# Kernel tuning notes

Hardware: AMD Instinct MI355X
Metric: run time of the kernel (lower is better)

Reference implementation:

```python
import jax, jax.numpy as jnp
import numpy as np

N_NODES = 100000
N_EDGES = 1600000
IN_FEATS = 16
HIDDEN = 100
OUT_FEATS = 3


def setup_inputs() -> dict:
    key = jax.random.key(0)
    ks = jax.random.split(key, 12)
    inp = {
        "x": jax.random.normal(ks[0], (N_NODES, IN_FEATS), dtype=jnp.float32),
        "edge_feats": jax.random.uniform(ks[1], (N_EDGES, 1), dtype=jnp.float32),
        "src": jax.random.randint(ks[2], (N_EDGES,), 0, N_NODES, dtype=jnp.int32),
        "dst": jax.random.randint(ks[3], (N_EDGES,), 0, N_NODES, dtype=jnp.int32),
        # lift: Linear(in_feats, hidden)
        "W_lift": jax.random.normal(ks[4], (IN_FEATS, HIDDEN), dtype=jnp.float32) / np.sqrt(IN_FEATS),
        "b_lift": jnp.zeros((HIDDEN,), dtype=jnp.float32),
        # three MPL layers: Linear(2*hidden, hidden)
        "W1": jax.random.normal(ks[5], (2 * HIDDEN, HIDDEN), dtype=jnp.float32) / np.sqrt(2 * HIDDEN),
        "b1": jnp.zeros((HIDDEN,), dtype=jnp.float32),
        "W2": jax.random.normal(ks[6], (2 * HIDDEN, HIDDEN), dtype=jnp.float32) / np.sqrt(2 * HIDDEN),
        "b2": jnp.zeros((HIDDEN,), dtype=jnp.float32),
        "W3": jax.random.normal(ks[7], (2 * HIDDEN, HIDDEN), dtype=jnp.float32) / np.sqrt(2 * HIDDEN),
        "b3": jnp.zeros((HIDDEN,), dtype=jnp.float32),
        # out: Linear(hidden, out_feats)
        "W_out": jax.random.normal(ks[8], (HIDDEN, OUT_FEATS), dtype=jnp.float32) / np.sqrt(HIDDEN),
        "b_out": jnp.zeros((OUT_FEATS,), dtype=jnp.float32),
    }
    return inp


def _mpl(h, edge_feats, src, dst, W, b):
    # gather src node feats, multiply by per-edge weight, scatter-sum to dst
    msg = h[src] * edge_feats                                # [E, H]
    reduced = jax.ops.segment_sum(msg, dst, num_segments=N_NODES)  # [N, H]
    return jax.nn.relu(jnp.concatenate([h, reduced], axis=-1) @ W + b)


def reference(x, edge_feats, src, dst, W_lift, b_lift, W1, b1, W2, b2, W3, b3, W_out, b_out):
    h = jnp.tanh(x @ W_lift + b_lift)          # [N, 100]
    h = _mpl(h, edge_feats, src, dst, W1, b1)
    h = _mpl(h, edge_feats, src, dst, W2, b2)
    h = _mpl(h, edge_feats, src, dst, W3, b3)
    return jax.nn.sigmoid(h @ W_out + b_out)   # [N, 3]
```

## Files before the change

kernel.cpp:

```cpp
#include <hip/hip_runtime.h>
#include <hip/hip_fp16.h>
#include <cstdint>
#include <cstddef>

#define NN 100000
#define NE 1600000
#define HID 100
#define INF 16

typedef _Float16 f16x8 __attribute__((ext_vector_type(8)));
typedef float f32x4 __attribute__((ext_vector_type(4)));

__device__ __forceinline__ float2 up_f16(unsigned int u) {
  __half2 h = *reinterpret_cast<const __half2*>(&u);
  return __half22float2(h);
}
__device__ __forceinline__ unsigned int pk_f16(float lo, float hi) {
  __half2 h = __floats2half2_rn(lo, hi);
  return *reinterpret_cast<const unsigned int*>(&h);
}
__device__ __forceinline__ f16x8 as_f16x8(uint4 v) {
  union { uint4 u; f16x8 f; } c; c.u = v; return c.f;
}

__global__ void k_hist(const int* __restrict__ dst, int* __restrict__ deg,
                       int* __restrict__ rank) {
  int e = blockIdx.x * 256 + threadIdx.x;
  if (e < NE) rank[e] = atomicAdd(&deg[dst[e]], 1);
}

__global__ void k_scan1(const int* __restrict__ deg, int* __restrict__ offs,
                        int* __restrict__ bsum) {
  __shared__ int s[256];
  int t = threadIdx.x;
  int i = blockIdx.x * 256 + t;
  int v = (i < NN) ? deg[i] : 0;
  s[t] = v; __syncthreads();
  for (int off = 1; off < 256; off <<= 1) {
    int x = (t >= off) ? s[t - off] : 0;
    __syncthreads();
    s[t] += x;
    __syncthreads();
  }
  if (i < NN) offs[i] = s[t] - v;
  if (t == 255) bsum[blockIdx.x] = s[255];
}

__global__ void k_scan2(int* __restrict__ bsum, int nb) {
  __shared__ int s[512];
  int t = threadIdx.x;
  int v = (t < nb) ? bsum[t] : 0;
  s[t] = v; __syncthreads();
  for (int off = 1; off < 512; off <<= 1) {
    int x = (t >= off) ? s[t - off] : 0;
    __syncthreads();
    s[t] += x;
    __syncthreads();
  }
  if (t < nb) bsum[t] = s[t] - v;
}

__global__ void k_scan3(int* __restrict__ offs, const int* __restrict__ bsum) {
  int i = blockIdx.x * 256 + threadIdx.x;
  if (i < NN) offs[i] += bsum[i >> 8];
  else if (i == NN) offs[NN] = NE;
}

__global__ void k_fill(const int* __restrict__ src, const int* __restrict__ dst,
                       const float* __restrict__ ef, const int* __restrict__ offs,
                       const int* __restrict__ rank,
                       unsigned long long* __restrict__ epack) {
  int e = blockIdx.x * 256 + threadIdx.x;
  if (e >= NE) return;
  int p = offs[dst[e]] + rank[e];
  unsigned long long v = (unsigned int)src[e] |
                         ((unsigned long long)(unsigned int)__float_as_int(ef[e]) << 32);
  epack[p] = v;
}

__device__ __forceinline__ float wval(const float* W, int kp, int col) {
  if (col >= HID) return 0.f;
  if (kp < 128) return (kp < 100) ? W[kp * HID + col] : 0.f;
  int k2 = kp - 128;
  return (k2 < 100) ? W[(100 + k2) * HID + col] : 0.f;
}
__global__ void k_wpack(const float* __restrict__ W, uint4* __restrict__ Bp) {
  int tid = blockIdx.x * 256 + threadIdx.x;
  if (tid >= 56 * 64) return;
  int lane = tid & 63, f = tid >> 6;
  int s = f / 7, n = f % 7;
  int col = n * 16 + (lane & 15);
  int kb = s * 32 + (lane >> 4) * 8;
  unsigned int u0 = pk_f16(wval(W, kb + 0, col), wval(W, kb + 1, col));
  unsigned int u1 = pk_f16(wval(W, kb + 2, col), wval(W, kb + 3, col));
  unsigned int u2 = pk_f16(wval(W, kb + 4, col), wval(W, kb + 5, col));
  unsigned int u3 = pk_f16(wval(W, kb + 6, col), wval(W, kb + 7, col));
  Bp[tid] = make_uint4(u0, u1, u2, u3);
}

__global__ __launch_bounds__(256) void k_lift(const float* __restrict__ x,
                                              const float* __restrict__ Wl,
                                              const float* __restrict__ bl,
                                              unsigned short* __restrict__ h16) {
  __shared__ uint2 sh[256][25];
  int t = threadIdx.x;
  int n = blockIdx.x * 256 + t;
  int nc = n < NN ? n : NN - 1;
  const float4* W4 = (const float4*)Wl;
  const float4* b4 = (const float4*)bl;
  float4 acc[25];
  #pragma unroll
  for (int j = 0; j < 25; ++j) acc[j] = b4[j];
  const float4* xr = (const float4*)(x + (size_t)nc * INF);
  for (int k4 = 0; k4 < 4; ++k4) {
    float4 xv = xr[k4];
    #pragma unroll
    for (int c = 0; c < 4; ++c) {
      float xs = (&xv.x)[c];
      int k = k4 * 4 + c;
      #pragma unroll
      for (int j = 0; j < 25; ++j) {
        acc[j].x = fmaf(xs, W4[k * 25 + j].x, acc[j].x);
        acc[j].y = fmaf(xs, W4[k * 25 + j].y, acc[j].y);
        acc[j].z = fmaf(xs, W4[k * 25 + j].z, acc[j].z);
        acc[j].w = fmaf(xs, W4[k * 25 + j].w, acc[j].w);
      }
    }
  }
  #pragma unroll
  for (int j = 0; j < 25; ++j) {
    float4 v = acc[j];
    sh[t][j] = make_uint2(pk_f16(tanhf(v.x), tanhf(v.y)),
                          pk_f16(tanhf(v.z), tanhf(v.w)));
  }
  __syncthreads();
  const uint4* shv = (const uint4*)sh;
  uint4* ov = (uint4*)h16;
  size_t gbase = (size_t)blockIdx.x * 3200;
  #pragma unroll
  for (int i = 0; i < 13; ++i) {
    int idx = i * 256 + t;
    if (idx < 3200 && gbase + idx < 1250000) ov[gbase + idx] = shv[idx];
  }
}

__global__ __launch_bounds__(256) void k_reduce(const unsigned short* __restrict__ h16,
                                                const int* __restrict__ offs,
                                                const int2* __restrict__ ep,
                                                unsigned int* __restrict__ red16) {
  int wid = (blockIdx.x * 256 + threadIdx.x) >> 6;
  int node = __builtin_amdgcn_readfirstlane(wid);
  int lane = threadIdx.x & 63;
  int lc = lane < 25 ? lane : 24;
  int beg = offs[node], end = offs[node + 1];
  const uint2* __restrict__ h2 = (const uint2*)h16;
  float4 acc = make_float4(0.f, 0.f, 0.f, 0.f);
  int i = beg;
  for (; i + 8 <= end; i += 8) {
    int2 e0 = ep[i + 0], e1 = ep[i + 1], e2 = ep[i + 2], e3 = ep[i + 3];
    int2 e4 = ep[i + 4], e5 = ep[i + 5], e6 = ep[i + 6], e7 = ep[i + 7];
    uint2 v0 = h2[(size_t)e0.x * 25 + lc];
    uint2 v1 = h2[(size_t)e1.x * 25 + lc];
    uint2 v2 = h2[(size_t)e2.x * 25 + lc];
    uint2 v3 = h2[(size_t)e3.x * 25 + lc];
    uint2 v4 = h2[(size_t)e4.x * 25 + lc];
    uint2 v5 = h2[(size_t)e5.x * 25 + lc];
    uint2 v6 = h2[(size_t)e6.x * 25 + lc];
    uint2 v7 = h2[(size_t)e7.x * 25 + lc];
    float w0 = __int_as_float(e0.y), w1 = __int_as_float(e1.y);
    float w2 = __int_as_float(e2.y), w3 = __int_as_float(e3.y);
    float w4 = __int_as_float(e4.y), w5 = __int_as_float(e5.y);
    float w6 = __int_as_float(e6.y), w7 = __int_as_float(e7.y);
    float2 a0 = up_f16(v0.x), b0 = up_f16(v0.y);
    float2 a1 = up_f16(v1.x), b1 = up_f16(v1.y);
    float2 a2 = up_f16(v2.x), b2 = up_f16(v2.y);
    float2 a3 = up_f16(v3.x), b3 = up_f16(v3.y);
    float2 a4 = up_f16(v4.x), b4 = up_f16(v4.y);
    float2 a5 = up_f16(v5.x), b5 = up_f16(v5.y);
    float2 a6 = up_f16(v6.x), b6 = up_f16(v6.y);
    float2 a7 = up_f16(v7.x), b7 = up_f16(v7.y);
    acc.x = fmaf(w0, a0.x, acc.x); acc.y = fmaf(w0, a0.y, acc.y);
    acc.z = fmaf(w0, b0.x, acc.z); acc.w = fmaf(w0, b0.y, acc.w);
    acc.x = fmaf(w1, a1.x, acc.x); acc.y = fmaf(w1, a1.y, acc.y);
    acc.z = fmaf(w1, b1.x, acc.z); acc.w = fmaf(w1, b1.y, acc.w);
    acc.x = fmaf(w2, a2.x, acc.x); acc.y = fmaf(w2, a2.y, acc.y);
    acc.z = fmaf(w2, b2.x, acc.z); acc.w = fmaf(w2, b2.y, acc.w);
    acc.x = fmaf(w3, a3.x, acc.x); acc.y = fmaf(w3, a3.y, acc.y);
    acc.z = fmaf(w3, b3.x, acc.z); acc.w = fmaf(w3, b3.y, acc.w);
    acc.x = fmaf(w4, a4.x, acc.x); acc.y = fmaf(w4, a4.y, acc.y);
    acc.z = fmaf(w4, b4.x, acc.z); acc.w = fmaf(w4, b4.y, acc.w);
    acc.x = fmaf(w5, a5.x, acc.x); acc.y = fmaf(w5, a5.y, acc.y);
    acc.z = fmaf(w5, b5.x, acc.z); acc.w = fmaf(w5, b5.y, acc.w);
    acc.x = fmaf(w6, a6.x, acc.x); acc.y = fmaf(w6, a6.y, acc.y);
    acc.z = fmaf(w6, b6.x, acc.z); acc.w = fmaf(w6, b6.y, acc.w);
    acc.x = fmaf(w7, a7.x, acc.x); acc.y = fmaf(w7, a7.y, acc.y);
    acc.z = fmaf(w7, b7.x, acc.z); acc.w = fmaf(w7, b7.y, acc.w);
  }
  for (; i + 4 <= end; i += 4) {
    int2 e0 = ep[i + 0], e1 = ep[i + 1], e2 = ep[i + 2], e3 = ep[i + 3];
    uint2 v0 = h2[(size_t)e0.x * 25 + lc];
    uint2 v1 = h2[(size_t)e1.x * 25 + lc];
    uint2 v2 = h2[(size_t)e2.x * 25 + lc];
    uint2 v3 = h2[(size_t)e3.x * 25 + lc];
    float w0 = __int_as_float(e0.y), w1 = __int_as_float(e1.y);
    float w2 = __int_as_float(e2.y), w3 = __int_as_float(e3.y);
    float2 a0 = up_f16(v0.x), b0 = up_f16(v0.y);
    float2 a1 = up_f16(v1.x), b1 = up_f16(v1.y);
    float2 a2 = up_f16(v2.x), b2 = up_f16(v2.y);
    float2 a3 = up_f16(v3.x), b3 = up_f16(v3.y);
    acc.x = fmaf(w0, a0.x, acc.x); acc.y = fmaf(w0, a0.y, acc.y);
    acc.z = fmaf(w0, b0.x, acc.z); acc.w = fmaf(w0, b0.y, acc.w);
    acc.x = fmaf(w1, a1.x, acc.x); acc.y = fmaf(w1, a1.y, acc.y);
    acc.z = fmaf(w1, b1.x, acc.z); acc.w = fmaf(w1, b1.y, acc.w);
    acc.x = fmaf(w2, a2.x, acc.x); acc.y = fmaf(w2, a2.y, acc.y);
    acc.z = fmaf(w2, b2.x, acc.z); acc.w = fmaf(w2, b2.y, acc.w);
    acc.x = fmaf(w3, a3.x, acc.x); acc.y = fmaf(w3, a3.y, acc.y);
    acc.z = fmaf(w3, b3.x, acc.z); acc.w = fmaf(w3, b3.y, acc.w);
  }
  for (; i < end; ++i) {
    int2 e0 = ep[i];
    uint2 v0 = h2[(size_t)e0.x * 25 + lc];
    float w0 = __int_as_float(e0.y);
    float2 a0 = up_f16(v0.x), b0 = up_f16(v0.y);
    acc.x = fmaf(w0, a0.x, acc.x); acc.y = fmaf(w0, a0.y, acc.y);
    acc.z = fmaf(w0, b0.x, acc.z); acc.w = fmaf(w0, b0.y, acc.w);
  }
  if (lane < 25) {
    ((uint2*)red16)[(size_t)node * 25 + lane] =
        make_uint2(pk_f16(acc.x, acc.y), pk_f16(acc.z, acc.w));
  }
}

__global__ __launch_bounds__(256) void k_mlp(const unsigned int* __restrict__ hp,
                                             const unsigned int* __restrict__ rp,
                                             const uint4* __restrict__ Bpk,
                                             const float* __restrict__ bias,
                                             unsigned short* __restrict__ out16) {
  __shared__ unsigned int xs[64 * 132];
  const int t = threadIdx.x;
  const int w = t >> 6, lane = t & 63;
  const int blk = blockIdx.x;
  const size_t base2 = (size_t)blk * 3200;
  const size_t limit2 = (size_t)NN * 50;

  for (int i = t; i < 64 * 28; i += 256) {
    int row = i / 28, c = i % 28;
    int col = (c < 14) ? (50 + c) : (100 + c);
    xs[row * 132 + col] = 0;
  }
  for (int i = t; i < 3200; i += 256) {
    int row = i / 50, c = i % 50;
    size_t g = base2 + i; if (g >= limit2) g = limit2 - 1;
    xs[row * 132 + c] = hp[g];
    xs[row * 132 + 64 + c] = rp[g];
  }
  __syncthreads();

  const int rowA = (w << 4) + (lane & 15);
  const int kg = lane >> 4;
  f32x4 acc[7];
  #pragma unroll
  for (int n = 0; n < 7; ++n) {
    int c = n * 16 + (lane & 15);
    float bv = (c < HID) ? bias[c] : 0.f;
    acc[n] = (f32x4){bv, bv, bv, bv};
  }
  const uint4* bp = Bpk + lane;
  #pragma unroll
  for (int s = 0; s < 8; ++s) {
    uint4 av = *reinterpret_cast<const uint4*>(&xs[rowA * 132 + s * 16 + kg * 4]);
    f16x8 af = as_f16x8(av);
    #pragma unroll
    for (int n = 0; n < 7; ++n) {
      f16x8 bf = as_f16x8(bp[(s * 7 + n) * 64]);
      acc[n] = __builtin_amdgcn_mfma_f32_16x16x32_f16(af, bf, acc[n], 0, 0, 0);
    }
  }
  const int orow0 = blk * 64 + (w << 4) + (kg << 2);
  const int ocol = lane & 15;
  #pragma unroll
  for (int n = 0; n < 7; ++n) {
    int c = n * 16 + ocol;
    if (c < HID) {
      #pragma unroll
      for (int q = 0; q < 4; ++q) {
        int rr = orow0 + q;
        if (rr < NN) {
          float v = fmaxf(acc[n][q], 0.f);
          out16[(size_t)rr * HID + c] = __half_as_ushort(__float2half(v));
        }
      }
    }
  }
}

__global__ __launch_bounds__(256) void k_out(const unsigned short* __restrict__ h16,
                                             const float* __restrict__ Wo,
                                             const float* __restrict__ bo,
                                             float* __restrict__ out) {
  int n = blockIdx.x * 256 + threadIdx.x;
  if (n >= NN) return;
  float a0 = bo[0], a1 = bo[1], a2 = bo[2];
  const uint2* hr = (const uint2*)(h16 + (size_t)n * HID);
  for (int k2 = 0; k2 < 25; ++k2) {
    uint2 v = hr[k2];
    float2 fa = up_f16(v.x), fb = up_f16(v.y);
    int k = k2 * 4;
    a0 = fmaf(fa.x, Wo[(k + 0) * 3 + 0], a0); a1 = fmaf(fa.x, Wo[(k + 0) * 3 + 1], a1); a2 = fmaf(fa.x, Wo[(k + 0) * 3 + 2], a2);
    a0 = fmaf(fa.y, Wo[(k + 1) * 3 + 0], a0); a1 = fmaf(fa.y, Wo[(k + 1) * 3 + 1], a1); a2 = fmaf(fa.y, Wo[(k + 1) * 3 + 2], a2);
    a0 = fmaf(fb.x, Wo[(k + 2) * 3 + 0], a0); a1 = fmaf(fb.x, Wo[(k + 2) * 3 + 1], a1); a2 = fmaf(fb.x, Wo[(k + 2) * 3 + 2], a2);
    a0 = fmaf(fb.y, Wo[(k + 3) * 3 + 0], a0); a1 = fmaf(fb.y, Wo[(k + 3) * 3 + 1], a1); a2 = fmaf(fb.y, Wo[(k + 3) * 3 + 2], a2);
  }
  out[(size_t)n * 3 + 0] = 1.f / (1.f + expf(-a0));
  out[(size_t)n * 3 + 1] = 1.f / (1.f + expf(-a1));
  out[(size_t)n * 3 + 2] = 1.f / (1.f + expf(-a2));
}

extern "C" void kernel_launch(void* const* d_in, const int* in_sizes, int n_in,
                              void* d_out, int out_size, void* d_ws, size_t ws_size,
                              hipStream_t stream) {
  const float* x  = (const float*)d_in[0];
  const float* ef = (const float*)d_in[1];
  const int*   src = (const int*)d_in[2];
  const int*   dst = (const int*)d_in[3];
  const float* Wl = (const float*)d_in[4];
  const float* bl = (const float*)d_in[5];
  const float* W1 = (const float*)d_in[6];
  const float* b1 = (const float*)d_in[7];
  const float* W2 = (const float*)d_in[8];
  const float* b2 = (const float*)d_in[9];
  const float* W3 = (const float*)d_in[10];
  const float* b3 = (const float*)d_in[11];
  const float* Wo = (const float*)d_in[12];
  const float* bo = (const float*)d_in[13];
  float* out = (float*)d_out;

  char* ws = (char*)d_ws;
  unsigned int*   red16  = (unsigned int*)(ws);
  uint4*          Wpk    = (uint4*)(ws + 20000000);
  unsigned short* hA16   = (unsigned short*)(ws + 40000000);
  unsigned short* hB16   = (unsigned short*)(ws + 60000000);
  int*            offs   = (int*)(ws + 80000000);
  int*            deg    = (int*)(ws + 80400128);
  unsigned long long* epack = (unsigned long long*)(ws + 80800256);
  int*            bsum   = (int*)(ws + 93600256);
  int*            rank   = (int*)ws;

  const int scanBlocks = (NN + 255) / 256;
  const int mlpBlocks  = (NN + 63) / 64;
  uint4* Wpk1 = Wpk;
  uint4* Wpk2 = Wpk + 3584;
  uint4* Wpk3 = Wpk + 7168;

  hipMemsetAsync(deg, 0, NN * sizeof(int), stream);
  k_hist <<<(NE + 255) / 256, 256, 0, stream>>>(dst, deg, rank);
  k_scan1<<<scanBlocks, 256, 0, stream>>>(deg, offs, bsum);
  k_scan2<<<1, 512, 0, stream>>>(bsum, scanBlocks);
  k_scan3<<<scanBlocks, 256, 0, stream>>>(offs, bsum);
  k_fill <<<(NE + 255) / 256, 256, 0, stream>>>(src, dst, ef, offs, rank, epack);

  k_wpack<<<14, 256, 0, stream>>>(W1, Wpk1);
  k_wpack<<<14, 256, 0, stream>>>(W2, Wpk2);
  k_wpack<<<14, 256, 0, stream>>>(W3, Wpk3);

  k_lift<<<scanBlocks, 256, 0, stream>>>(x, Wl, bl, hA16);

  k_reduce<<<NN / 4, 256, 0, stream>>>(hA16, offs, (const int2*)epack, red16);
  k_mlp   <<<mlpBlocks, 256, 0, stream>>>((const unsigned int*)hA16, red16, Wpk1, b1, hB16);

  k_reduce<<<NN / 4, 256, 0, stream>>>(hB16, offs, (const int2*)epack, red16);
  k_mlp   <<<mlpBlocks, 256, 0, stream>>>((const unsigned int*)hB16, red16, Wpk2, b2, hA16);

  k_reduce<<<NN / 4, 256, 0, stream>>>(hA16, offs, (const int2*)epack, red16);
  k_mlp   <<<mlpBlocks, 256, 0, stream>>>((const unsigned int*)hA16, red16, Wpk3, b3, hB16);

  k_out<<<scanBlocks, 256, 0, stream>>>(hB16, Wo, bo, out);
}
```

Before: 511.6 us.

## Fuse neighbor aggregation into MLP layer kernel and fold output head

Moves the per-node gather/scale/sum aggregation into the MLP kernel, writing the reduced features straight into shared memory instead of round-tripping them through global memory. The last layer also applies the output linear and sigmoid in-kernel, and the three weight-pack launches become one. This removes the intermediate red16 buffer and several launches. The cost is fewer waves per node (each wave serially handles 16 nodes) and less parallelism during the gather phase, so latency hiding for the random gathers may suffer.

```diff
diff --git a/kernel.cpp b/kernel.cpp
--- a/kernel.cpp
+++ b/kernel.cpp
@@ -84,10 +84,13 @@
   int k2 = kp - 128;
   return (k2 < 100) ? W[(100 + k2) * HID + col] : 0.f;
 }
-__global__ void k_wpack(const float* __restrict__ W, uint4* __restrict__ Bp) {
+__global__ void k_wpack3(const float* __restrict__ W1, const float* __restrict__ W2,
+                         const float* __restrict__ W3, uint4* __restrict__ Bp) {
   int tid = blockIdx.x * 256 + threadIdx.x;
-  if (tid >= 56 * 64) return;
-  int lane = tid & 63, f = tid >> 6;
+  if (tid >= 3 * 3584) return;
+  int l = tid / 3584, r = tid % 3584;
+  const float* W = (l == 0) ? W1 : (l == 1) ? W2 : W3;
+  int lane = r & 63, f = r >> 6;
   int s = f / 7, n = f % 7;
   int col = n * 16 + (lane & 15);
   int kb = s * 32 + (lane >> 4) * 8;
@@ -144,104 +147,16 @@
   }
 }
 
-__global__ __launch_bounds__(256) void k_reduce(const unsigned short* __restrict__ h16,
-                                                const int* __restrict__ offs,
-                                                const int2* __restrict__ ep,
-                                                unsigned int* __restrict__ red16) {
-  int wid = (blockIdx.x * 256 + threadIdx.x) >> 6;
-  int node = __builtin_amdgcn_readfirstlane(wid);
-  int lane = threadIdx.x & 63;
-  int lc = lane < 25 ? lane : 24;
-  int beg = offs[node], end = offs[node + 1];
-  const uint2* __restrict__ h2 = (const uint2*)h16;
-  float4 acc = make_float4(0.f, 0.f, 0.f, 0.f);
-  int i = beg;
-  for (; i + 8 <= end; i += 8) {
-    int2 e0 = ep[i + 0], e1 = ep[i + 1], e2 = ep[i + 2], e3 = ep[i + 3];
-    int2 e4 = ep[i + 4], e5 = ep[i + 5], e6 = ep[i + 6], e7 = ep[i + 7];
-    uint2 v0 = h2[(size_t)e0.x * 25 + lc];
-    uint2 v1 = h2[(size_t)e1.x * 25 + lc];
-    uint2 v2 = h2[(size_t)e2.x * 25 + lc];
-    uint2 v3 = h2[(size_t)e3.x * 25 + lc];
-    uint2 v4 = h2[(size_t)e4.x * 25 + lc];
-    uint2 v5 = h2[(size_t)e5.x * 25 + lc];
-    uint2 v6 = h2[(size_t)e6.x * 25 + lc];
-    uint2 v7 = h2[(size_t)e7.x * 25 + lc];
-    float w0 = __int_as_float(e0.y), w1 = __int_as_float(e1.y);
-    float w2 = __int_as_float(e2.y), w3 = __int_as_float(e3.y);
-    float w4 = __int_as_float(e4.y), w5 = __int_as_float(e5.y);
-    float w6 = __int_as_float(e6.y), w7 = __int_as_float(e7.y);
-    float2 a0 = up_f16(v0.x), b0 = up_f16(v0.y);
-    float2 a1 = up_f16(v1.x), b1 = up_f16(v1.y);
-    float2 a2 = up_f16(v2.x), b2 = up_f16(v2.y);
-    float2 a3 = up_f16(v3.x), b3 = up_f16(v3.y);
-    float2 a4 = up_f16(v4.x), b4 = up_f16(v4.y);
-    float2 a5 = up_f16(v5.x), b5 = up_f16(v5.y);
-    float2 a6 = up_f16(v6.x), b6 = up_f16(v6.y);
-    float2 a7 = up_f16(v7.x), b7 = up_f16(v7.y);
-    acc.x = fmaf(w0, a0.x, acc.x); acc.y = fmaf(w0, a0.y, acc.y);
-    acc.z = fmaf(w0, b0.x, acc.z); acc.w = fmaf(w0, b0.y, acc.w);
-    acc.x = fmaf(w1, a1.x, acc.x); acc.y = fmaf(w1, a1.y, acc.y);
-    acc.z = fmaf(w1, b1.x, acc.z); acc.w = fmaf(w1, b1.y, acc.w);
-    acc.x = fmaf(w2, a2.x, acc.x); acc.y = fmaf(w2, a2.y, acc.y);
-    acc.z = fmaf(w2, b2.x, acc.z); acc.w = fmaf(w2, b2.y, acc.w);
-    acc.x = fmaf(w3, a3.x, acc.x); acc.y = fmaf(w3, a3.y, acc.y);
-    acc.z = fmaf(w3, b3.x, acc.z); acc.w = fmaf(w3, b3.y, acc.w);
-    acc.x = fmaf(w4, a4.x, acc.x); acc.y = fmaf(w4, a4.y, acc.y);
-    acc.z = fmaf(w4, b4.x, acc.z); acc.w = fmaf(w4, b4.y, acc.w);
-    acc.x = fmaf(w5, a5.x, acc.x); acc.y = fmaf(w5, a5.y, acc.y);
-    acc.z = fmaf(w5, b5.x, acc.z); acc.w = fmaf(w5, b5.y, acc.w);
-    acc.x = fmaf(w6, a6.x, acc.x); acc.y = fmaf(w6, a6.y, acc.y);
-    acc.z = fmaf(w6, b6.x, acc.z); acc.w = fmaf(w6, b6.y, acc.w);
-    acc.x = fmaf(w7, a7.x, acc.x); acc.y = fmaf(w7, a7.y, acc.y);
-    acc.z = fmaf(w7, b7.x, acc.z); acc.w = fmaf(w7, b7.y, acc.w);
-  }
-  for (; i + 4 <= end; i += 4) {
-    int2 e0 = ep[i + 0], e1 = ep[i + 1], e2 = ep[i + 2], e3 = ep[i + 3];
-    uint2 v0 = h2[(size_t)e0.x * 25 + lc];
-    uint2 v1 = h2[(size_t)e1.x * 25 + lc];
-    uint2 v2 = h2[(size_t)e2.x * 25 + lc];
-    uint2 v3 = h2[(size_t)e3.x * 25 + lc];
-    float w0 = __int_as_float(e0.y), w1 = __int_as_float(e1.y);
-    float w2 = __int_as_float(e2.y), w3 = __int_as_float(e3.y);
-    float2 a0 = up_f16(v0.x), b0 = up_f16(v0.y);
-    float2 a1 = up_f16(v1.x), b1 = up_f16(v1.y);
-    float2 a2 = up_f16(v2.x), b2 = up_f16(v2.y);
-    float2 a3 = up_f16(v3.x), b3 = up_f16(v3.y);
-    acc.x = fmaf(w0, a0.x, acc.x); acc.y = fmaf(w0, a0.y, acc.y);
-    acc.z = fmaf(w0, b0.x, acc.z); acc.w = fmaf(w0, b0.y, acc.w);
-    acc.x = fmaf(w1, a1.x, acc.x); acc.y = fmaf(w1, a1.y, acc.y);
-    acc.z = fmaf(w1, b1.x, acc.z); acc.w = fmaf(w1, b1.y, acc.w);
-    acc.x = fmaf(w2, a2.x, acc.x); acc.y = fmaf(w2, a2.y, acc.y);
-    acc.z = fmaf(w2, b2.x, acc.z); acc.w = fmaf(w2, b2.y, acc.w);
-    acc.x = fmaf(w3, a3.x, acc.x); acc.y = fmaf(w3, a3.y, acc.y);
-    acc.z = fmaf(w3, b3.x, acc.z); acc.w = fmaf(w3, b3.y, acc.w);
-  }
-  for (; i < end; ++i) {
-    int2 e0 = ep[i];
-    uint2 v0 = h2[(size_t)e0.x * 25 + lc];
-    float w0 = __int_as_float(e0.y);
-    float2 a0 = up_f16(v0.x), b0 = up_f16(v0.y);
-    acc.x = fmaf(w0, a0.x, acc.x); acc.y = fmaf(w0, a0.y, acc.y);
-    acc.z = fmaf(w0, b0.x, acc.z); acc.w = fmaf(w0, b0.y, acc.w);
-  }
-  if (lane < 25) {
-    ((uint2*)red16)[(size_t)node * 25 + lane] =
-        make_uint2(pk_f16(acc.x, acc.y), pk_f16(acc.z, acc.w));
-  }
-}
-
-__global__ __launch_bounds__(256) void k_mlp(const unsigned int* __restrict__ hp,
-                                             const unsigned int* __restrict__ rp,
-                                             const uint4* __restrict__ Bpk,
-                                             const float* __restrict__ bias,
-                                             unsigned short* __restrict__ out16) {
-  __shared__ unsigned int xs[64 * 132];
-  const int t = threadIdx.x;
-  const int w = t >> 6, lane = t & 63;
-  const int blk = blockIdx.x;
+__device__ __forceinline__ void layer_core(const unsigned short* __restrict__ h16,
+                                           const int* __restrict__ offs,
+                                           const int2* __restrict__ ep,
+                                           const uint4* __restrict__ Bpk,
+                                           const float* __restrict__ bias,
+                                           unsigned int* xs, f32x4 (&acc)[7],
+                                           int t, int w, int lane, int blk) {
   const size_t base2 = (size_t)blk * 3200;
   const size_t limit2 = (size_t)NN * 50;
+  const unsigned int* hp = (const unsigned int*)h16;
 
   for (int i = t; i < 64 * 28; i += 256) {
     int row = i / 28, c = i % 28;
@@ -252,13 +167,74 @@
     int row = i / 50, c = i % 50;
     size_t g = base2 + i; if (g >= limit2) g = limit2 - 1;
     xs[row * 132 + c] = hp[g];
-    xs[row * 132 + 64 + c] = rp[g];
+  }
+
+  const uint2* __restrict__ h2 = (const uint2*)h16;
+  int lc = lane < 25 ? lane : 24;
+  for (int j = 0; j < 16; ++j) {
+    int gn = blk * 64 + (w << 4) + j;
+    int node = __builtin_amdgcn_readfirstlane(gn < NN ? gn : NN - 1);
+    int beg = offs[node], end = offs[node + 1];
+    float4 a = make_float4(0.f, 0.f, 0.f, 0.f);
+    int i = beg;
+    for (; i + 8 <= end; i += 8) {
+      int2 e0 = ep[i + 0], e1 = ep[i + 1], e2 = ep[i + 2], e3 = ep[i + 3];
+      int2 e4 = ep[i + 4], e5 = ep[i + 5], e6 = ep[i + 6], e7 = ep[i + 7];
+      uint2 v0 = h2[(size_t)e0.x * 25 + lc];
+      uint2 v1 = h2[(size_t)e1.x * 25 + lc];
+      uint2 v2 = h2[(size_t)e2.x * 25 + lc];
+      uint2 v3 = h2[(size_t)e3.x * 25 + lc];
+      uint2 v4 = h2[(size_t)e4.x * 25 + lc];
+      uint2 v5 = h2[(size_t)e5.x * 25 + lc];
+      uint2 v6 = h2[(size_t)e6.x * 25 + lc];
+      uint2 v7 = h2[(size_t)e7.x * 25 + lc];
+      float w0 = __int_as_float(e0.y), w1 = __int_as_float(e1.y);
+      float w2 = __int_as_float(e2.y), w3 = __int_as_float(e3.y);
+      float w4 = __int_as_float(e4.y), w5 = __int_as_float(e5.y);
+      float w6 = __int_as_float(e6.y), w7 = __int_as_float(e7.y);
+      float2 a0 = up_f16(v0.x), b0 = up_f16(v0.y);
+      float2 a1 = up_f16(v1.x), b1 = up_f16(v1.y);
+      float2 a2 = up_f16(v2.x), b2 = up_f16(v2.y);
+      float2 a3 = up_f16(v3.x), b3 = up_f16(v3.y);
+      float2 a4 = up_f16(v4.x), b4 = up_f16(v4.y);
+      float2 a5 = up_f16(v5.x), b5 = up_f16(v5.y);
+      float2 a6 = up_f16(v6.x), b6 = up_f16(v6.y);
+      float2 a7 = up_f16(v7.x), b7 = up_f16(v7.y);
+      a.x = fmaf(w0, a0.x, a.x); a.y = fmaf(w0, a0.y, a.y);
+      a.z = fmaf(w0, b0.x, a.z); a.w = fmaf(w0, b0.y, a.w);
+      a.x = fmaf(w1, a1.x, a.x); a.y = fmaf(w1, a1.y, a.y);
+      a.z = fmaf(w1, b1.x, a.z); a.w = fmaf(w1, b1.y, a.w);
+      a.x = fmaf(w2, a2.x, a.x); a.y = fmaf(w2, a2.y, a.y);
+      a.z = fmaf(w2, b2.x, a.z); a.w = fmaf(w2, b2.y, a.w);
+      a.x = fmaf(w3, a3.x, a.x); a.y = fmaf(w3, a3.y, a.y);
+      a.z = fmaf(w3, b3.x, a.z); a.w = fmaf(w3, b3.y, a.w);
+      a.x = fmaf(w4, a4.x, a.x); a.y = fmaf(w4, a4.y, a.y);
+      a.z = fmaf(w4, b4.x, a.z); a.w = fmaf(w4, b4.y, a.w);
+      a.x = fmaf(w5, a5.x, a.x); a.y = fmaf(w5, a5.y, a.y);
+      a.z = fmaf(w5, b5.x, a.z); a.w = fmaf(w5, b5.y, a.w);
+      a.x = fmaf(w6, a6.x, a.x); a.y = fmaf(w6, a6.y, a.y);
+      a.z = fmaf(w6, b6.x, a.z); a.w = fmaf(w6, b6.y, a.w);
+      a.x = fmaf(w7, a7.x, a.x); a.y = fmaf(w7, a7.y, a.y);
+      a.z = fmaf(w7, b7.x, a.z); a.w = fmaf(w7, b7.y, a.w);
+    }
+    for (; i < end; ++i) {
+      int2 e0 = ep[i];
+      uint2 v0 = h2[(size_t)e0.x * 25 + lc];
+      float w0 = __int_as_float(e0.y);
+      float2 a0 = up_f16(v0.x), b0 = up_f16(v0.y);
+      a.x = fmaf(w0, a0.x, a.x); a.y = fmaf(w0, a0.y, a.y);
+      a.z = fmaf(w0, b0.x, a.z); a.w = fmaf(w0, b0.y, a.w);
+    }
+    if (lane < 25) {
+      int row = (w << 4) + j;
+      xs[row * 132 + 64 + 2 * lc] = pk_f16(a.x, a.y);
+      xs[row * 132 + 64 + 2 * lc + 1] = pk_f16(a.z, a.w);
+    }
   }
   __syncthreads();
 
   const int rowA = (w << 4) + (lane & 15);
   const int kg = lane >> 4;
-  f32x4 acc[7];
   #pragma unroll
   for (int n = 0; n < 7; ++n) {
     int c = n * 16 + (lane & 15);
@@ -276,6 +252,22 @@
       acc[n] = __builtin_amdgcn_mfma_f32_16x16x32_f16(af, bf, acc[n], 0, 0, 0);
     }
   }
+}
+
+__global__ __launch_bounds__(256) void k_layer(const unsigned short* __restrict__ h16,
+                                               const int* __restrict__ offs,
+                                               const int2* __restrict__ ep,
+                                               const uint4* __restrict__ Bpk,
+                                               const float* __restrict__ bias,
+                                               unsigned short* __restrict__ out16) {
+  __shared__ unsigned int xs[64 * 132];
+  const int t = threadIdx.x;
+  const int w = t >> 6, lane = t & 63;
+  const int blk = blockIdx.x;
+  f32x4 acc[7];
+  layer_core(h16, offs, ep, Bpk, bias, xs, acc, t, w, lane, blk);
+
+  const int kg = lane >> 4;
   const int orow0 = blk * 64 + (w << 4) + (kg << 2);
   const int ocol = lane & 15;
   #pragma unroll
@@ -294,26 +286,55 @@
   }
 }
 
-__global__ __launch_bounds__(256) void k_out(const unsigned short* __restrict__ h16,
-                                             const float* __restrict__ Wo,
-                                             const float* __restrict__ bo,
-                                             float* __restrict__ out) {
-  int n = blockIdx.x * 256 + threadIdx.x;
-  if (n >= NN) return;
-  float a0 = bo[0], a1 = bo[1], a2 = bo[2];
-  const uint2* hr = (const uint2*)(h16 + (size_t)n * HID);
-  for (int k2 = 0; k2 < 25; ++k2) {
-    uint2 v = hr[k2];
-    float2 fa = up_f16(v.x), fb = up_f16(v.y);
-    int k = k2 * 4;
-    a0 = fmaf(fa.x, Wo[(k + 0) * 3 + 0], a0); a1 = fmaf(fa.x, Wo[(k + 0) * 3 + 1], a1); a2 = fmaf(fa.x, Wo[(k + 0) * 3 + 2], a2);
-    a0 = fmaf(fa.y, Wo[(k + 1) * 3 + 0], a0); a1 = fmaf(fa.y, Wo[(k + 1) * 3 + 1], a1); a2 = fmaf(fa.y, Wo[(k + 1) * 3 + 2], a2);
-    a0 = fmaf(fb.x, Wo[(k + 2) * 3 + 0], a0); a1 = fmaf(fb.x, Wo[(k + 2) * 3 + 1], a1); a2 = fmaf(fb.x, Wo[(k + 2) * 3 + 2], a2);
-    a0 = fmaf(fb.y, Wo[(k + 3) * 3 + 0], a0); a1 = fmaf(fb.y, Wo[(k + 3) * 3 + 1], a1); a2 = fmaf(fb.y, Wo[(k + 3) * 3 + 2], a2);
-  }
-  out[(size_t)n * 3 + 0] = 1.f / (1.f + expf(-a0));
-  out[(size_t)n * 3 + 1] = 1.f / (1.f + expf(-a1));
-  out[(size_t)n * 3 + 2] = 1.f / (1.f + expf(-a2));
+__global__ __launch_bounds__(256) void k_layer_out(const unsigned short* __restrict__ h16,
+                                                   const int* __restrict__ offs,
+                                                   const int2* __restrict__ ep,
+                                                   const uint4* __restrict__ Bpk,
+                                                   const float* __restrict__ bias,
+                                                   const float* __restrict__ Wo,
+                                                   const float* __restrict__ bo,
+                                                   float* __restrict__ out) {
+  __shared__ unsigned int xs[64 * 132];
+  const int t = threadIdx.x;
+  const int w = t >> 6, lane = t & 63;
+  const int blk = blockIdx.x;
+  f32x4 acc[7];
+  layer_core(h16, offs, ep, Bpk, bias, xs, acc, t, w, lane, blk);
+  __syncthreads();
+
+  float* xf = (float*)xs;
+  const int kg = lane >> 4;
+  const int orl = (w << 4) + (kg << 2);
+  const int ocol = lane & 15;
+  #pragma unroll
+  for (int n = 0; n < 7; ++n) {
+    int c = n * 16 + ocol;
+    if (c < HID) {
+      #pragma unroll
+      for (int q = 0; q < 4; ++q) xf[(orl + q) * 104 + c] = fmaxf(acc[n][q], 0.f);
+    }
+  }
+  __syncthreads();
+
+  int row = t >> 2, seg = t & 3;
+  int gn = blk * 64 + row;
+  float s0 = 0.f, s1 = 0.f, s2 = 0.f;
+  int cbase = seg * 25;
+  #pragma unroll
+  for (int k = 0; k < 25; ++k) {
+    float v = xf[row * 104 + cbase + k];
+    s0 = fmaf(v, Wo[(cbase + k) * 3 + 0], s0);
+    s1 = fmaf(v, Wo[(cbase + k) * 3 + 1], s1);
+    s2 = fmaf(v, Wo[(cbase + k) * 3 + 2], s2);
+  }
+  s0 += __shfl_xor(s0, 1); s0 += __shfl_xor(s0, 2);
+  s1 += __shfl_xor(s1, 1); s1 += __shfl_xor(s1, 2);
+  s2 += __shfl_xor(s2, 1); s2 += __shfl_xor(s2, 2);
+  if (seg == 0 && gn < NN) {
+    out[(size_t)gn * 3 + 0] = 1.f / (1.f + expf(-(s0 + bo[0])));
+    out[(size_t)gn * 3 + 1] = 1.f / (1.f + expf(-(s1 + bo[1])));
+    out[(size_t)gn * 3 + 2] = 1.f / (1.f + expf(-(s2 + bo[2])));
+  }
 }
 
 extern "C" void kernel_launch(void* const* d_in, const int* in_sizes, int n_in,
@@ -336,7 +357,7 @@
   float* out = (float*)d_out;
 
   char* ws = (char*)d_ws;
-  unsigned int*   red16  = (unsigned int*)(ws);
+  int*            rank   = (int*)ws;
   uint4*          Wpk    = (uint4*)(ws + 20000000);
   unsigned short* hA16   = (unsigned short*)(ws + 40000000);
   unsigned short* hB16   = (unsigned short*)(ws + 60000000);
@@ -344,13 +365,9 @@
   int*            deg    = (int*)(ws + 80400128);
   unsigned long long* epack = (unsigned long long*)(ws + 80800256);
   int*            bsum   = (int*)(ws + 93600256);
-  int*            rank   = (int*)ws;
-
-  const int scanBlocks = (NN + 255) / 256;
-  const int mlpBlocks  = (NN + 63) / 64;
-  uint4* Wpk1 = Wpk;
-  uint4* Wpk2 = Wpk + 3584;
-  uint4* Wpk3 = Wpk + 7168;
+
+  const int scanBlocks  = (NN + 255) / 256;
+  const int layerBlocks = (NN + 63) / 64;
 
   hipMemsetAsync(deg, 0, NN * sizeof(int), stream);
   k_hist <<<(NE + 255) / 256, 256, 0, stream>>>(dst, deg, rank);
@@ -359,20 +376,14 @@
   k_scan3<<<scanBlocks, 256, 0, stream>>>(offs, bsum);
   k_fill <<<(NE + 255) / 256, 256, 0, stream>>>(src, dst, ef, offs, rank, epack);
 
-  k_wpack<<<14, 256, 0, stream>>>(W1, Wpk1);
-  k_wpack<<<14, 256, 0, stream>>>(W2, Wpk2);
-  k_wpack<<<14, 256, 0, stream>>>(W3, Wpk3);
+  k_wpack3<<<42, 256, 0, stream>>>(W1, W2, W3, Wpk);
 
   k_lift<<<scanBlocks, 256, 0, stream>>>(x, Wl, bl, hA16);
 
-  k_reduce<<<NN / 4, 256, 0, stream>>>(hA16, offs, (const int2*)epack, red16);
-  k_mlp   <<<mlpBlocks, 256, 0, stream>>>((const unsigned int*)hA16, red16, Wpk1, b1, hB16);
-
-  k_reduce<<<NN / 4, 256, 0, stream>>>(hB16, offs, (const int2*)epack, red16);
-  k_mlp   <<<mlpBlocks, 256, 0, stream>>>((const unsigned int*)hB16, red16, Wpk2, b2, hA16);
-
-  k_reduce<<<NN / 4, 256, 0, stream>>>(hA16, offs, (const int2*)epack, red16);
-  k_mlp   <<<mlpBlocks, 256, 0, stream>>>((const unsigned int*)hA16, red16, Wpk3, b3, hB16);
-
-  k_out<<<scanBlocks, 256, 0, stream>>>(hB16, Wo, bo, out);
-}
+  k_layer    <<<layerBlocks, 256, 0, stream>>>(hA16, offs, (const int2*)epack,
+                                               Wpk, b1, hB16);
+  k_layer    <<<layerBlocks, 256, 0, stream>>>(hB16, offs, (const int2*)epack,
+                                               Wpk + 3584, b2, hA16);
+  k_layer_out<<<layerBlocks, 256, 0, stream>>>(hA16, offs, (const int2*)epack,
+                                               Wpk + 7168, b3, Wo, bo, out);
+}
```

New measurement: 619.8 us. 1.21x slower.
